# Kernel optimization log

Measured on AMD Instinct MI355X. Metric: run time of the kernel, lower is better.

Reference implementation:

```python
import jax, jax.numpy as jnp
import numpy as np

N, M = 50000, 32
F_NODE, F_EDGE = 64, 64


def setup_inputs() -> dict:
    key = jax.random.key(0)
    k1, k2, k3, k4, k5 = jax.random.split(key, 5)
    node_in_fea = jax.random.normal(k1, (N, F_NODE), dtype=jnp.float32)
    edge_fea = jax.random.normal(k2, (N, M, F_EDGE), dtype=jnp.float32)
    # indices in [-1, N); -1 marks invalid neighbor (masked out), as in the torch code
    edge_fea_idx = jax.random.randint(k3, (N, M), -1, N)
    # fc_full: Linear(2*F_NODE + F_EDGE -> 2*F_NODE), kaiming-uniform-ish init
    fan_in = 2 * F_NODE + F_EDGE
    bound = float(np.sqrt(6.0 / fan_in))
    W = jax.random.uniform(k4, (2 * F_NODE, fan_in), minval=-bound, maxval=bound, dtype=jnp.float32)
    b = jnp.zeros((2 * F_NODE,), dtype=jnp.float32)
    alpha = jnp.float32(0.7)
    return {"node_in_fea": node_in_fea, "edge_fea": edge_fea,
            "edge_fea_idx": edge_fea_idx, "W": W, "b": b, "alpha": alpha}


def softplus(x):
    return jax.nn.softplus(x)


def reference(node_in_fea, edge_fea, edge_fea_idx, W, b, alpha):
    n, m = edge_fea_idx.shape
    # gather neighbor node features; clip -1 -> 0 (result is masked to zero below,
    # matching torch where idx=-1 wraps but contribution is zeroed by the mask)
    safe_idx = jnp.clip(edge_fea_idx, 0)
    node_edge_fea = node_in_fea[safe_idx]                       # (N, M, F)
    self_fea = jnp.broadcast_to(node_in_fea[:, None, :], (n, m, node_in_fea.shape[-1]))
    total_nbr_fea = jnp.concatenate([self_fea, node_edge_fea, edge_fea], axis=2)  # (N, M, 2F+Fe)
    total_gated_fea = jnp.einsum('nmf,of->nmo', total_nbr_fea, W) + b             # (N, M, 2F)
    nbr_filter, nbr_core = jnp.split(total_gated_fea, 2, axis=2)
    mask = (edge_fea_idx >= 0).astype(nbr_filter.dtype)[:, :, None]
    nbr_filter = jax.nn.sigmoid(nbr_filter) * mask
    nbr_core = softplus(nbr_core) * mask
    nbr_sumed = jnp.sum(nbr_filter * nbr_core, axis=1)          # (N, F)
    out = softplus(alpha * node_in_fea + nbr_sumed)
    return out
```

## Files before the change

kernel.cpp:

```cpp
#include <hip/hip_runtime.h>
#include <hip/hip_bf16.h>

#define MNBR 32
#define FDIM 64

typedef __attribute__((ext_vector_type(8))) short bf16x8;
typedef __attribute__((ext_vector_type(4))) float f32x4;
typedef __attribute__((ext_vector_type(4))) float fvec4;

static __device__ __forceinline__ unsigned short f2bf(float x) {
    unsigned u = __builtin_bit_cast(unsigned, x);
    u += 0x7FFFu + ((u >> 16) & 1u);
    return (unsigned short)(u >> 16);
}
static __device__ __forceinline__ bf16x8 pack8(fvec4 a, fvec4 b) {
    bf16x8 r;
    r[0] = (short)f2bf(a[0]); r[1] = (short)f2bf(a[1]);
    r[2] = (short)f2bf(a[2]); r[3] = (short)f2bf(a[3]);
    r[4] = (short)f2bf(b[0]); r[5] = (short)f2bf(b[1]);
    r[6] = (short)f2bf(b[2]); r[7] = (short)f2bf(b[3]);
    return r;
}
static __device__ __forceinline__ float sigmoid_f(float x) {
    return __builtin_amdgcn_rcpf(1.f + __expf(-x));
}
static __device__ __forceinline__ float softplus_f(float x) {
    return fmaxf(x, 0.f) + __logf(1.f + __expf(-fabsf(x)));
}

__global__ __launch_bounds__(256) void precompute_ab_mfma(
    const float* __restrict__ node, const float* __restrict__ W,
    const float* __restrict__ b, float* __restrict__ A, float* __restrict__ B,
    int n_nodes)
{
    const int lane = threadIdx.x & 63;
    const int w    = threadIdx.x >> 6;
    const int rt   = blockIdx.x * 4 + w;
    const int ntiles = (n_nodes + 15) / 16;
    if (rt >= ntiles) return;
    const int c = lane & 15, g = lane >> 4;

    bf16x8 af[2];
    {
        const float* p = node + (size_t)(rt * 16 + c) * FDIM + g * 8;
        fvec4 e0 = *(const fvec4*)(p);
        fvec4 e1 = *(const fvec4*)(p + 4);
        fvec4 e2 = *(const fvec4*)(p + 32);
        fvec4 e3 = *(const fvec4*)(p + 36);
        af[0] = pack8(e0, e1);
        af[1] = pack8(e2, e3);
    }
    for (int t = 0; t < 16; ++t) {
        const int o = t * 16 + c;
        f32x4 acc = {0.f, 0.f, 0.f, 0.f};
        #pragma unroll
        for (int s = 0; s < 2; ++s) {
            const float* wp = (o < 128)
                ? W + (size_t)o * 192 + s * 32 + g * 8
                : W + (size_t)(o - 128) * 192 + 64 + s * 32 + g * 8;
            fvec4 w0 = *(const fvec4*)(wp);
            fvec4 w1 = *(const fvec4*)(wp + 4);
            bf16x8 bfr = pack8(w0, w1);
            acc = __builtin_amdgcn_mfma_f32_16x16x32_bf16(af[s], bfr, acc, 0, 0, 0);
        }
        const float bias = (o < 128) ? b[o] : 0.f;
        #pragma unroll
        for (int r = 0; r < 4; ++r) {
            int n = rt * 16 + g * 4 + r;
            float v = acc[r] + bias;
            if (o < 128) A[(size_t)n * 128 + o] = v;
            else         B[(size_t)n * 128 + (o - 128)] = v;
        }
    }
}

__global__ __launch_bounds__(256) void edge_mfma(
    const float* __restrict__ node, const float* __restrict__ edge,
    const int* __restrict__ eidx, const float* __restrict__ W,
    const float* __restrict__ Atab, const float* __restrict__ Btab,
    const float* __restrict__ alphap, float* __restrict__ out, int n_nodes)
{
    const int lane = threadIdx.x & 63;
    const int w    = threadIdx.x >> 6;
    const int wid  = blockIdx.x * 4 + w;
    const int c = lane & 15, g = lane >> 4;
    const float alpha = alphap[0];

    bf16x8 Wf[8][2];
    #pragma unroll
    for (int t = 0; t < 8; ++t) {
        const float* wr = W + (size_t)(t * 16 + c) * 192 + 128 + g * 8;
        fvec4 w0 = *(const fvec4*)(wr);
        fvec4 w1 = *(const fvec4*)(wr + 4);
        fvec4 w2 = *(const fvec4*)(wr + 32);
        fvec4 w3 = *(const fvec4*)(wr + 36);
        Wf[t][0] = pack8(w0, w1);
        Wf[t][1] = pack8(w2, w3);
    }

    for (int nn = 0; nn < 2; ++nn) {
        const int n = wid * 2 + nn;
        if (n >= n_nodes) break;

        float a_f[8];
        #pragma unroll
        for (int t = 0; t < 8; ++t)
            a_f[t] = Atab[(size_t)n * 128 + t * 16 + c];

        float nsum[4] = {0.f, 0.f, 0.f, 0.f};

        #pragma unroll
        for (int half = 0; half < 2; ++half) {
            bf16x8 ea[2];
            {
                const float* p = edge + ((size_t)n * MNBR + half * 16 + c) * FDIM + g * 8;
                fvec4 e0 = __builtin_nontemporal_load((const fvec4*)(p));
                fvec4 e1 = __builtin_nontemporal_load((const fvec4*)(p + 4));
                fvec4 e2 = __builtin_nontemporal_load((const fvec4*)(p + 32));
                fvec4 e3 = __builtin_nontemporal_load((const fvec4*)(p + 36));
                ea[0] = pack8(e0, e1);
                ea[1] = pack8(e2, e3);
            }
            f32x4 acc[8];
            #pragma unroll
            for (int t = 0; t < 8; ++t) acc[t] = (f32x4){0.f, 0.f, 0.f, 0.f};
            #pragma unroll
            for (int s = 0; s < 2; ++s)
                #pragma unroll
                for (int t = 0; t < 8; ++t)
                    acc[t] = __builtin_amdgcn_mfma_f32_16x16x32_bf16(ea[s], Wf[t][s], acc[t], 0, 0, 0);

            const int4 jv = *(const int4*)(eidx + (size_t)n * MNBR + half * 16 + g * 4);
            #pragma unroll
            for (int r = 0; r < 4; ++r) {
                const int j = (r == 0) ? jv.x : (r == 1) ? jv.y : (r == 2) ? jv.z : jv.w;
                if (j < 0) continue;
                const float* bp = Btab + (size_t)j * 128 + c;
                #pragma unroll
                for (int t = 0; t < 4; ++t) {
                    float gf = acc[t][r]     + a_f[t]     + bp[t * 16];
                    float gc = acc[t + 4][r] + a_f[t + 4] + bp[t * 16 + 64];
                    nsum[t] += sigmoid_f(gf) * softplus_f(gc);
                }
            }
        }

        #pragma unroll
        for (int t = 0; t < 4; ++t) {
            nsum[t] += __shfl_xor(nsum[t], 16);
            nsum[t] += __shfl_xor(nsum[t], 32);
        }
        float v = nsum[0];
        v = (g == 1) ? nsum[1] : v;
        v = (g == 2) ? nsum[2] : v;
        v = (g == 3) ? nsum[3] : v;
        float x = fmaf(alpha, node[(size_t)n * FDIM + lane], v);
        out[(size_t)n * FDIM + lane] = softplus_f(x);
    }
}

extern "C" void kernel_launch(void* const* d_in, const int* in_sizes, int n_in,
                              void* d_out, int out_size, void* d_ws, size_t ws_size,
                              hipStream_t stream) {
    const float* node  = (const float*)d_in[0];
    const float* edge  = (const float*)d_in[1];
    const int*   eidx  = (const int*)d_in[2];
    const float* W     = (const float*)d_in[3];
    const float* b     = (const float*)d_in[4];
    const float* alpha = (const float*)d_in[5];
    float* out = (float*)d_out;

    const int n_nodes = in_sizes[0] / FDIM;

    float* A = (float*)d_ws;
    float* B = A + (size_t)n_nodes * 128;

    const int ntiles = (n_nodes + 15) / 16;
    precompute_ab_mfma<<<(ntiles + 3) / 4, 256, 0, stream>>>(node, W, b, A, B, n_nodes);

    const int nwaves = (n_nodes + 1) / 2;
    edge_mfma<<<(nwaves + 3) / 4, 256, 0, stream>>>(node, edge, eidx, W, A, B,
                                                    alpha, out, n_nodes);
}
```

Measured before the change: 771.1 us.

## Gather bf16 neighbor features into edge MFMA instead of precomputed neighbor projections

```diff
diff --git a/kernel.cpp b/kernel.cpp
--- a/kernel.cpp
+++ b/kernel.cpp
@@ -5,6 +5,7 @@
 #define FDIM 64
 
 typedef __attribute__((ext_vector_type(8))) short bf16x8;
+typedef __attribute__((ext_vector_type(16))) float f32x16;
 typedef __attribute__((ext_vector_type(4))) float f32x4;
 typedef __attribute__((ext_vector_type(4))) float fvec4;
 
@@ -28,134 +29,142 @@
     return fmaxf(x, 0.f) + __logf(1.f + __expf(-fabsf(x)));
 }
 
-__global__ __launch_bounds__(256) void precompute_ab_mfma(
+__global__ __launch_bounds__(256) void prep_kernel(
     const float* __restrict__ node, const float* __restrict__ W,
-    const float* __restrict__ b, float* __restrict__ A, float* __restrict__ B,
-    int n_nodes)
+    const float* __restrict__ b, float* __restrict__ A_pk,
+    short* __restrict__ nodeBF, short* __restrict__ Wfrag, int n_nodes)
 {
     const int lane = threadIdx.x & 63;
     const int w    = threadIdx.x >> 6;
-    const int rt   = blockIdx.x * 4 + w;
-    const int ntiles = (n_nodes + 15) / 16;
-    if (rt >= ntiles) return;
     const int c = lane & 15, g = lane >> 4;
 
-    bf16x8 af[2];
-    {
-        const float* p = node + (size_t)(rt * 16 + c) * FDIM + g * 8;
+    if (blockIdx.x == 0) {
+        const int c32 = lane & 31, hi = lane >> 5;
+        for (int fi = w; fi < 32; fi += 4) {
+            int t = fi >> 3, s = fi & 7;
+            int o = t * 32 + c32;
+            int kcol = (s < 4) ? (128 + s * 16 + hi * 8)
+                               : (64 + (s - 4) * 16 + hi * 8);
+            const float* wp = W + (size_t)o * 192 + kcol;
+            bf16x8 fr;
+            #pragma unroll
+            for (int j = 0; j < 8; ++j) fr[j] = (short)f2bf(wp[j]);
+            *(bf16x8*)(Wfrag + ((size_t)fi * 64 + lane) * 8) = fr;
+        }
+    }
+
+    bf16x8 Wsf[8][2];
+    float bias[8];
+    #pragma unroll
+    for (int t = 0; t < 8; ++t) {
+        const int o = t * 16 + c;
+        bias[t] = b[o];
+        #pragma unroll
+        for (int s = 0; s < 2; ++s) {
+            const float* wp = W + (size_t)o * 192 + s * 32 + g * 8;
+            fvec4 w0 = *(const fvec4*)(wp);
+            fvec4 w1 = *(const fvec4*)(wp + 4);
+            Wsf[t][s] = pack8(w0, w1);
+        }
+    }
+
+    const int ntiles = (n_nodes + 15) >> 4;
+    for (int rt = blockIdx.x * 4 + w; rt < ntiles; rt += gridDim.x * 4) {
+        const int row = rt * 16 + c;
+        const float* p = node + (size_t)row * FDIM + g * 8;
         fvec4 e0 = *(const fvec4*)(p);
         fvec4 e1 = *(const fvec4*)(p + 4);
         fvec4 e2 = *(const fvec4*)(p + 32);
         fvec4 e3 = *(const fvec4*)(p + 36);
-        af[0] = pack8(e0, e1);
-        af[1] = pack8(e2, e3);
-    }
-    for (int t = 0; t < 16; ++t) {
-        const int o = t * 16 + c;
-        f32x4 acc = {0.f, 0.f, 0.f, 0.f};
+        bf16x8 af0 = pack8(e0, e1);
+        bf16x8 af1 = pack8(e2, e3);
+        *(bf16x8*)(nodeBF + (size_t)row * FDIM + g * 8)      = af0;
+        *(bf16x8*)(nodeBF + (size_t)row * FDIM + 32 + g * 8) = af1;
+
+        f32x4 acc[8];
         #pragma unroll
-        for (int s = 0; s < 2; ++s) {
-            const float* wp = (o < 128)
-                ? W + (size_t)o * 192 + s * 32 + g * 8
-                : W + (size_t)(o - 128) * 192 + 64 + s * 32 + g * 8;
-            fvec4 w0 = *(const fvec4*)(wp);
-            fvec4 w1 = *(const fvec4*)(wp + 4);
-            bf16x8 bfr = pack8(w0, w1);
-            acc = __builtin_amdgcn_mfma_f32_16x16x32_bf16(af[s], bfr, acc, 0, 0, 0);
+        for (int t = 0; t < 8; ++t) acc[t] = (f32x4){0.f, 0.f, 0.f, 0.f};
+        #pragma unroll
+        for (int t = 0; t < 8; ++t) {
+            acc[t] = __builtin_amdgcn_mfma_f32_16x16x32_bf16(af0, Wsf[t][0], acc[t], 0, 0, 0);
+            acc[t] = __builtin_amdgcn_mfma_f32_16x16x32_bf16(af1, Wsf[t][1], acc[t], 0, 0, 0);
         }
-        const float bias = (o < 128) ? b[o] : 0.f;
         #pragma unroll
-        for (int r = 0; r < 4; ++r) {
-            int n = rt * 16 + g * 4 + r;
-            float v = acc[r] + bias;
-            if (o < 128) A[(size_t)n * 128 + o] = v;
-            else         B[(size_t)n * 128 + (o - 128)] = v;
+        for (int t = 0; t < 8; ++t) {
+            const int o = t * 16 + c;
+            const size_t base = ((size_t)(o & 31)) * 4 + (o >> 5);
+            #pragma unroll
+            for (int r = 0; r < 4; ++r) {
+                int n = rt * 16 + g * 4 + r;
+                A_pk[(size_t)n * 128 + base] = acc[t][r] + bias[t];
+            }
         }
     }
 }
 
-__global__ __launch_bounds__(256) void edge_mfma(
+__global__ __launch_bounds__(256) void edge_fused(
     const float* __restrict__ node, const float* __restrict__ edge,
-    const int* __restrict__ eidx, const float* __restrict__ W,
-    const float* __restrict__ Atab, const float* __restrict__ Btab,
+    const int* __restrict__ eidx, const float* __restrict__ A_pk,
+    const short* __restrict__ nodeBF, const short* __restrict__ Wfrag,
     const float* __restrict__ alphap, float* __restrict__ out, int n_nodes)
 {
+    __shared__ short sW[32 * 64 * 8];
+    for (int i = threadIdx.x; i < 32 * 64; i += 256)
+        *(bf16x8*)(sW + (size_t)i * 8) = *(const bf16x8*)(Wfrag + (size_t)i * 8);
+    __syncthreads();
+
     const int lane = threadIdx.x & 63;
     const int w    = threadIdx.x >> 6;
-    const int wid  = blockIdx.x * 4 + w;
-    const int c = lane & 15, g = lane >> 4;
+    const int c32 = lane & 31, hi = lane >> 5;
     const float alpha = alphap[0];
 
-    bf16x8 Wf[8][2];
-    #pragma unroll
-    for (int t = 0; t < 8; ++t) {
-        const float* wr = W + (size_t)(t * 16 + c) * 192 + 128 + g * 8;
-        fvec4 w0 = *(const fvec4*)(wr);
-        fvec4 w1 = *(const fvec4*)(wr + 4);
-        fvec4 w2 = *(const fvec4*)(wr + 32);
-        fvec4 w3 = *(const fvec4*)(wr + 36);
-        Wf[t][0] = pack8(w0, w1);
-        Wf[t][1] = pack8(w2, w3);
-    }
+    for (int n = blockIdx.x * 4 + w; n < n_nodes; n += gridDim.x * 4) {
+        const int j = eidx[(size_t)n * MNBR + c32];
+        const int jsafe = (j < 0) ? 0 : j;
 
-    for (int nn = 0; nn < 2; ++nn) {
-        const int n = wid * 2 + nn;
-        if (n >= n_nodes) break;
+        const fvec4 aq = *(const fvec4*)(A_pk + (size_t)n * 128 + c32 * 4);
+        const float ns = node[(size_t)n * FDIM + lane];
 
-        float a_f[8];
+        const float* ep = edge + ((size_t)n * MNBR + c32) * FDIM + hi * 8;
+        bf16x8 ea[4];
         #pragma unroll
-        for (int t = 0; t < 8; ++t)
-            a_f[t] = Atab[(size_t)n * 128 + t * 16 + c];
+        for (int s = 0; s < 4; ++s) {
+            fvec4 x0 = __builtin_nontemporal_load((const fvec4*)(ep + s * 16));
+            fvec4 x1 = __builtin_nontemporal_load((const fvec4*)(ep + s * 16 + 4));
+            ea[s] = pack8(x0, x1);
+        }
+        const short* np_ = nodeBF + (size_t)jsafe * FDIM + hi * 8;
+        bf16x8 na[4];
+        #pragma unroll
+        for (int s = 0; s < 4; ++s)
+            na[s] = *(const bf16x8*)(np_ + s * 16);
 
-        float nsum[4] = {0.f, 0.f, 0.f, 0.f};
-
+        f32x16 acc[4] = {};
         #pragma unroll
-        for (int half = 0; half < 2; ++half) {
-            bf16x8 ea[2];
-            {
-                const float* p = edge + ((size_t)n * MNBR + half * 16 + c) * FDIM + g * 8;
-                fvec4 e0 = __builtin_nontemporal_load((const fvec4*)(p));
-                fvec4 e1 = __builtin_nontemporal_load((const fvec4*)(p + 4));
-                fvec4 e2 = __builtin_nontemporal_load((const fvec4*)(p + 32));
-                fvec4 e3 = __builtin_nontemporal_load((const fvec4*)(p + 36));
-                ea[0] = pack8(e0, e1);
-                ea[1] = pack8(e2, e3);
-            }
-            f32x4 acc[8];
+        for (int s = 0; s < 8; ++s) {
+            const bf16x8 afr = (s < 4) ? ea[s] : na[s - 4];
             #pragma unroll
-            for (int t = 0; t < 8; ++t) acc[t] = (f32x4){0.f, 0.f, 0.f, 0.f};
-            #pragma unroll
-            for (int s = 0; s < 2; ++s)
-                #pragma unroll
-                for (int t = 0; t < 8; ++t)
-                    acc[t] = __builtin_amdgcn_mfma_f32_16x16x32_bf16(ea[s], Wf[t][s], acc[t], 0, 0, 0);
-
-            const int4 jv = *(const int4*)(eidx + (size_t)n * MNBR + half * 16 + g * 4);
-            #pragma unroll
-            for (int r = 0; r < 4; ++r) {
-                const int j = (r == 0) ? jv.x : (r == 1) ? jv.y : (r == 2) ? jv.z : jv.w;
-                if (j < 0) continue;
-                const float* bp = Btab + (size_t)j * 128 + c;
-                #pragma unroll
-                for (int t = 0; t < 4; ++t) {
-                    float gf = acc[t][r]     + a_f[t]     + bp[t * 16];
-                    float gc = acc[t + 4][r] + a_f[t + 4] + bp[t * 16 + 64];
-                    nsum[t] += sigmoid_f(gf) * softplus_f(gc);
-                }
+            for (int t = 0; t < 4; ++t) {
+                bf16x8 wf = *(const bf16x8*)(sW + ((size_t)(t * 8 + s) * 64 + lane) * 8);
+                acc[t] = __builtin_amdgcn_mfma_f32_32x32x16_bf16(afr, wf, acc[t], 0, 0, 0);
             }
         }
 
+        float nsum0 = 0.f, nsum1 = 0.f;
         #pragma unroll
-        for (int t = 0; t < 4; ++t) {
-            nsum[t] += __shfl_xor(nsum[t], 16);
-            nsum[t] += __shfl_xor(nsum[t], 32);
+        for (int r = 0; r < 16; ++r) {
+            const int row = (r & 3) + 8 * (r >> 2) + 4 * hi;
+            const int jr = __shfl(j, row, 32);
+            const float m = (jr >= 0) ? 1.f : 0.f;
+            float gf0 = acc[0][r] + aq[0], gc0 = acc[2][r] + aq[2];
+            float gf1 = acc[1][r] + aq[1], gc1 = acc[3][r] + aq[3];
+            nsum0 += m * (sigmoid_f(gf0) * softplus_f(gc0));
+            nsum1 += m * (sigmoid_f(gf1) * softplus_f(gc1));
         }
-        float v = nsum[0];
-        v = (g == 1) ? nsum[1] : v;
-        v = (g == 2) ? nsum[2] : v;
-        v = (g == 3) ? nsum[3] : v;
-        float x = fmaf(alpha, node[(size_t)n * FDIM + lane], v);
-        out[(size_t)n * FDIM + lane] = softplus_f(x);
+        nsum0 += __shfl_xor(nsum0, 32);
+        nsum1 += __shfl_xor(nsum1, 32);
+        const float v = hi ? nsum1 : nsum0;
+        out[(size_t)n * FDIM + lane] = softplus_f(fmaf(alpha, ns, v));
     }
 }
 
@@ -172,13 +181,15 @@
 
     const int n_nodes = in_sizes[0] / FDIM;
 
-    float* A = (float*)d_ws;
-    float* B = A + (size_t)n_nodes * 128;
+    char* ws = (char*)d_ws;
+    short* nodeBF = (short*)ws;
+    float* A_pk   = (float*)(ws + (size_t)n_nodes * FDIM * 2);
+    short* Wfrag  = (short*)(ws + (size_t)n_nodes * FDIM * 2
+                                + (size_t)n_nodes * 128 * 4);
 
-    const int ntiles = (n_nodes + 15) / 16;
-    precompute_ab_mfma<<<(ntiles + 3) / 4, 256, 0, stream>>>(node, W, b, A, B, n_nodes);
-
-    const int nwaves = (n_nodes + 1) / 2;
-    edge_mfma<<<(nwaves + 3) / 4, 256, 0, stream>>>(node, edge, eidx, W, A, B,
-                                                    alpha, out, n_nodes);
+    const int ntiles = (n_nodes + 15) >> 4;
+    prep_kernel<<<(ntiles + 3) / 4, 256, 0, stream>>>(node, W, b, A_pk, nodeBF,
+                                                      Wfrag, n_nodes);
+    edge_fused<<<2048, 256, 0, stream>>>(node, edge, eidx, A_pk, nodeBF, Wfrag,
+                                         alpha, out, n_nodes);
 }
```

Measured after the change: 781.0 us. About the same (+1.3%).
